# Kernel tuning notes

Measured on AMD Instinct MI355X. Metric: run time of the kernel, lower is better.

Reference implementation:

```python
import jax, jax.numpy as jnp
import numpy as np

T = 8192        # total tokens
HID = 2048      # hidden_size
H = 16          # num heads
D = 128         # head_dim
INNER = H * D   # 2048
CHUNK = 128
EPS = 1e-5
SCALE = D ** -0.5
ROPE_BASE = 600000.0


def _rmsnorm(x, w, eps=EPS):
    # x: [..., d]
    var = jnp.mean(jnp.square(x), axis=-1, keepdims=True)
    return x * jax.lax.rsqrt(var + eps) * w


def _rope(x, positions):
    # neox-style rope on full head_dim. x: [T, H, D], positions: [T]
    half = D // 2
    inv_freq = 1.0 / (ROPE_BASE ** (jnp.arange(half, dtype=jnp.float32) / half))
    ang = positions.astype(jnp.float32)[:, None] * inv_freq          # [T, half]
    cos = jnp.cos(ang)[:, None, :]                                   # [T, 1, half]
    sin = jnp.sin(ang)[:, None, :]
    x1, x2 = x[..., :half], x[..., half:]
    return jnp.concatenate([x1 * cos - x2 * sin, x2 * cos + x1 * sin], axis=-1)


def setup_inputs() -> dict:
    key = jax.random.key(0)
    ks = jax.random.split(key, 5)
    hidden_states = jax.random.normal(ks[0], (T, HID), dtype=jnp.float32)
    positions = jnp.arange(T, dtype=jnp.int64 if jax.config.jax_enable_x64 else jnp.int32)
    Wqkv = jax.random.normal(ks[1], (HID, 3 * INNER), dtype=jnp.float32) * 0.02
    q_ln_w = jnp.ones((D,), dtype=jnp.float32)
    k_ln_w = jnp.ones((D,), dtype=jnp.float32)
    Wg = jax.random.normal(ks[2], (HID, INNER), dtype=jnp.float32) * 0.02
    g_norm_w = jnp.ones((INNER,), dtype=jnp.float32)
    Wo = jax.random.normal(ks[3], (INNER, HID), dtype=jnp.float32) * 0.02
    return {"hidden_states": hidden_states, "positions": positions, "Wqkv": Wqkv,
            "q_ln_w": q_ln_w, "k_ln_w": k_ln_w, "Wg": Wg,
            "g_norm_w": g_norm_w, "Wo": Wo}


def reference(hidden_states, positions, Wqkv, q_ln_w, k_ln_w, Wg, g_norm_w, Wo):
    x = hidden_states.astype(jnp.float32)
    qkv = jax.nn.silu(x @ Wqkv)                                  # linear_silu=True, fp32
    q, k, v = jnp.split(qkv, [INNER, 2 * INNER], axis=-1)
    # per-head QK RMSNorm
    q = _rmsnorm(q.reshape(T, H, D), q_ln_w)
    k = _rmsnorm(k.reshape(T, H, D), k_ln_w)
    # rope
    q = _rope(q, positions)
    k = _rope(k, positions)
    v = v.reshape(T, H, D)
    q = q * SCALE  # scaling passed to RadixAttention

    # chunked causal linear attention: o_t = q_t @ sum_{s<=t} k_s v_s^T
    N = T // CHUNK
    qc = q.reshape(N, CHUNK, H, D)
    kc = k.reshape(N, CHUNK, H, D)
    vc = v.reshape(N, CHUNK, H, D)
    mask = jnp.tril(jnp.ones((CHUNK, CHUNK), dtype=jnp.float32))  # causal within chunk

    def step(S, chunk):
        qi, ki, vi = chunk                                        # [C, H, D]
        scores = jnp.einsum('chd,shd->hcs', qi, ki) * mask        # intra-chunk causal
        o = jnp.einsum('hcs,shd->chd', scores, vi)
        o = o + jnp.einsum('chd,hde->che', qi, S)                 # inter-chunk state
        S = S + jnp.einsum('chd,che->hde', ki, vi)
        return S, o

    S0 = jnp.zeros((H, D, D), dtype=jnp.float32)
    _, o = jax.lax.scan(step, S0, (qc, kc, vc))                   # o: [N, C, H, D]
    o = o.reshape(T, INNER)

    gate = x @ Wg                                                 # g_proj
    normed = _rmsnorm(o, g_norm_w)                                # group_norm_size == 1
    gated = jax.nn.sigmoid(gate) * normed
    return gated @ Wo                                             # out proj (no bias)
```

## Files before the change

kernel.cpp:

```cpp
#include <hip/hip_runtime.h>
#include <cstdint>
#include <cstddef>

typedef unsigned short u16;
typedef __attribute__((ext_vector_type(8))) short short8;
typedef __attribute__((ext_vector_type(4))) float f32x4;

#define T_SEQ 8192
#define NH 16
#define HD 128
#define NCH 64
#define KDIM 2048

constexpr float EPS = 1e-5f;
constexpr float SCALE = 0.08838834764831845f;

__device__ __forceinline__ u16 f2bf(float f) {
  union { float f; unsigned u; } v; v.f = f;
  unsigned r = v.u + 0x7fffu + ((v.u >> 16) & 1u);
  return (u16)(r >> 16);
}
__device__ __forceinline__ float bf2f(u16 h) {
  union { unsigned u; float f; } v; v.u = ((unsigned)h) << 16;
  return v.f;
}
__device__ __forceinline__ f32x4 mfma16(short8 a, short8 b, f32x4 c) {
  return __builtin_amdgcn_mfma_f32_16x16x32_bf16(a, b, c, 0, 0, 0);
}
__device__ __forceinline__ void gl2lds(const u16* g, u16* l) {
  __builtin_amdgcn_global_load_lds(
      (const __attribute__((address_space(1))) void*)g,
      (__attribute__((address_space(3))) void*)l, 16, 0, 0);
}

__global__ __launch_bounds__(256) void cast_f32_bf16(const float* __restrict__ src,
                                                     u16* __restrict__ dst, long n) {
  long i = ((long)blockIdx.x * 256 + threadIdx.x) * 8;
  if (i >= n) return;
  float4 a = *(const float4*)(src + i);
  float4 b = *(const float4*)(src + i + 4);
  alignas(16) u16 u[8] = {f2bf(a.x), f2bf(a.y), f2bf(a.z), f2bf(a.w),
                          f2bf(b.x), f2bf(b.y), f2bf(b.z), f2bf(b.w)};
  *(int4*)(dst + i) = *(const int4*)u;
}

__global__ __launch_bounds__(256) void transpose_cast(const float* __restrict__ W,
                                                      u16* __restrict__ Wt, int K, int N) {
  __shared__ u16 tile[64][72];
  int n0 = blockIdx.x * 64, k0 = blockIdx.y * 64;
  int tx = threadIdx.x, ty = threadIdx.y;
  for (int r = ty; r < 64; r += 4)
    tile[r][tx] = f2bf(W[(size_t)(k0 + r) * N + n0 + tx]);
  __syncthreads();
  for (int r = ty; r < 64; r += 4)
    Wt[(size_t)(n0 + r) * K + k0 + tx] = tile[tx][r];
}

template <int EPI>
__global__ __launch_bounds__(512) void gemm256(const u16* __restrict__ A,
                                               const u16* __restrict__ Bt, int N,
                                               float* __restrict__ Cf,
                                               u16* __restrict__ Cb,
                                               u16* __restrict__ q_t,
                                               u16* __restrict__ k_t,
                                               u16* __restrict__ v_t) {
  __shared__ u16 lds[65536];
  const int tid  = threadIdx.x;
  const int wave = tid >> 6, lane = tid & 63;
  const int lr = lane & 15, lg = lane >> 4;
  const int wr = wave >> 2, wc = wave & 3;
  const int bm = blockIdx.y, bn = blockIdx.x;
  const int sx  = (lr & 7) << 4;
  const int cu0 = ((lg * 16) ^ sx) >> 1;
  const int cu1 = ((64 + lg * 16) ^ sx) >> 1;

  const int srow  = tid >> 3;
  const int sslot = (tid & 7) ^ (srow & 7);
  const u16* gA = A  + (size_t)(bm * 256 + srow) * KDIM + sslot * 8;
  const u16* gB = Bt + (size_t)(bn * 256 + srow) * KDIM + sslot * 8;
  const int sbase = wave * 512;

  f32x4 acc[8][4];
  #pragma unroll
  for (int i = 0; i < 8; i++)
    #pragma unroll
    for (int j = 0; j < 4; j++) acc[i][j] = (f32x4){0.f, 0.f, 0.f, 0.f};

  auto STAGE = [&](int op, int buf, int half, int kt) {
    const u16* g = (op ? gB : gA) + (size_t)half * 128 * KDIM + kt * 64;
    u16* l = &lds[buf * 32768 + op * 16384 + half * 8192 + sbase];
    gl2lds(g, l);
    gl2lds(g + (size_t)64 * KDIM, l + 4096);
  };

  const int aoff = (wr * 64 + lr) * 64;
  const int boff = 16384 + (wc * 32 + lr) * 64;

  STAGE(0, 0, 0, 0); STAGE(1, 0, 0, 0); STAGE(0, 0, 1, 0); STAGE(1, 0, 1, 0);
  STAGE(0, 1, 0, 1); STAGE(1, 1, 1, 1); STAGE(0, 1, 1, 1);
  asm volatile("s_waitcnt vmcnt(6)" ::: "memory");
  __builtin_amdgcn_s_barrier();

  short8 af[4][2], b0f[2][2], b1f[2][2];
  const int NT = KDIM / 64;
  for (int t = 0; t < NT; ++t) {
    const int cur = t & 1, nxt = cur ^ 1;
    const int cb = cur * 32768;
    #pragma unroll
    for (int i = 0; i < 4; i++) {
      af[i][0] = *(const short8*)&lds[cb + aoff + i * 1024 + cu0];
      af[i][1] = *(const short8*)&lds[cb + aoff + i * 1024 + cu1];
    }
    #pragma unroll
    for (int j = 0; j < 2; j++) {
      b0f[j][0] = *(const short8*)&lds[cb + boff + j * 1024 + cu0];
      b0f[j][1] = *(const short8*)&lds[cb + boff + j * 1024 + cu1];
    }
    if (t + 1 < NT) STAGE(1, nxt, 0, t + 1);
    __builtin_amdgcn_s_barrier();
    asm volatile("s_waitcnt lgkmcnt(0)" ::: "memory");
    __builtin_amdgcn_s_setprio(1);
    #pragma unroll
    for (int i = 0; i < 4; i++)
      #pragma unroll
      for (int j = 0; j < 2; j++) {
        acc[i][j] = mfma16(af[i][0], b0f[j][0], acc[i][j]);
        acc[i][j] = mfma16(af[i][1], b0f[j][1], acc[i][j]);
      }
    __builtin_amdgcn_s_setprio(0);
    __builtin_amdgcn_s_barrier();
    #pragma unroll
    for (int j = 0; j < 2; j++) {
      b1f[j][0] = *(const short8*)&lds[cb + 8192 + boff + j * 1024 + cu0];
      b1f[j][1] = *(const short8*)&lds[cb + 8192 + boff + j * 1024 + cu1];
    }
    if (t + 2 < NT) STAGE(0, cur, 0, t + 2);
    __builtin_amdgcn_s_barrier();
    asm volatile("s_waitcnt lgkmcnt(0)" ::: "memory");
    __builtin_amdgcn_s_setprio(1);
    #pragma unroll
    for (int i = 0; i < 4; i++)
      #pragma unroll
      for (int j = 0; j < 2; j++) {
        acc[i][2 + j] = mfma16(af[i][0], b1f[j][0], acc[i][2 + j]);
        acc[i][2 + j] = mfma16(af[i][1], b1f[j][1], acc[i][2 + j]);
      }
    __builtin_amdgcn_s_setprio(0);
    __builtin_amdgcn_s_barrier();
    #pragma unroll
    for (int i = 0; i < 4; i++) {
      af[i][0] = *(const short8*)&lds[cb + 8192 + aoff + i * 1024 + cu0];
      af[i][1] = *(const short8*)&lds[cb + 8192 + aoff + i * 1024 + cu1];
    }
    if (t + 2 < NT) STAGE(1, cur, 1, t + 2);
    __builtin_amdgcn_s_barrier();
    asm volatile("s_waitcnt lgkmcnt(0)" ::: "memory");
    __builtin_amdgcn_s_setprio(1);
    #pragma unroll
    for (int i = 0; i < 4; i++)
      #pragma unroll
      for (int j = 0; j < 2; j++) {
        acc[4 + i][2 + j] = mfma16(af[i][0], b1f[j][0], acc[4 + i][2 + j]);
        acc[4 + i][2 + j] = mfma16(af[i][1], b1f[j][1], acc[4 + i][2 + j]);
      }
    __builtin_amdgcn_s_setprio(0);
    __builtin_amdgcn_s_barrier();
    if (t + 2 < NT) STAGE(0, cur, 1, t + 2);
    __builtin_amdgcn_s_barrier();
    asm volatile("s_waitcnt lgkmcnt(0)" ::: "memory");
    __builtin_amdgcn_s_setprio(1);
    #pragma unroll
    for (int i = 0; i < 4; i++)
      #pragma unroll
      for (int j = 0; j < 2; j++) {
        acc[4 + i][j] = mfma16(af[i][0], b0f[j][0], acc[4 + i][j]);
        acc[4 + i][j] = mfma16(af[i][1], b0f[j][1], acc[4 + i][j]);
      }
    __builtin_amdgcn_s_setprio(0);
    if (t + 2 < NT) asm volatile("s_waitcnt vmcnt(6)" ::: "memory");
    else            asm volatile("s_waitcnt vmcnt(0)" ::: "memory");
    __builtin_amdgcn_s_barrier();
  }

  #pragma unroll
  for (int mi = 0; mi < 8; mi++)
    #pragma unroll
    for (int nj = 0; nj < 4; nj++)
      #pragma unroll
      for (int r = 0; r < 4; r++) {
        int row = bm * 256 + (mi >> 2) * 128 + wr * 64 + (mi & 3) * 16 + lg * 4 + r;
        int col = bn * 256 + (nj >> 1) * 128 + wc * 32 + (nj & 1) * 16 + lr;
        float v = acc[mi][nj][r];
        if (EPI == 0) {
          Cf[(size_t)row * N + col] = v;
        } else if (EPI == 1) {
          Cb[(size_t)row * N + col] = f2bf(v);
        } else {
          float s = v / (1.0f + __expf(-v));
          int part = col >> 11;
          int h = (col >> 7) & 15;
          int d = col & 127;
          u16* dst = part == 0 ? q_t : (part == 1 ? k_t : v_t);
          dst[((size_t)h * T_SEQ + row) * HD + d] = f2bf(s);
        }
      }
}

__global__ __launch_bounds__(128) void qk_prep(u16* __restrict__ q_t, u16* __restrict__ k_t,
                                               const int* __restrict__ positions,
                                               const float* __restrict__ q_ln_w,
                                               const float* __restrict__ k_ln_w) {
  const int t = blockIdx.x, h = blockIdx.y, d = threadIdx.x;
  const size_t base = ((size_t)h * T_SEQ + t) * HD + d;
  float qv = bf2f(q_t[base]), kv = bf2f(k_t[base]);
  float s1 = qv * qv, s2 = kv * kv;
  #pragma unroll
  for (int off = 32; off > 0; off >>= 1) {
    s1 += __shfl_xor(s1, off);
    s2 += __shfl_xor(s2, off);
  }
  __shared__ float sh[4];
  if ((d & 63) == 0) { sh[(d >> 6) * 2] = s1; sh[(d >> 6) * 2 + 1] = s2; }
  __syncthreads();
  s1 = sh[0] + sh[2];
  s2 = sh[1] + sh[3];
  float rq = rsqrtf(s1 * (1.0f / 128.0f) + EPS);
  float rk = rsqrtf(s2 * (1.0f / 128.0f) + EPS);
  float qn = qv * rq * q_ln_w[d];
  float kn = kv * rk * k_ln_w[d];
  __shared__ float qsh[128], ksh[128];
  qsh[d] = qn; ksh[d] = kn;
  __syncthreads();
  int i = d & 63;
  float invf = exp2f((float)i * (-19.194593f / 64.0f));
  float ang = (float)positions[t] * invf;
  float cv = cosf(ang), sv = sinf(ang);
  float q2 = qsh[d ^ 64], k2 = ksh[d ^ 64];
  float qr = (d < 64) ? (qn * cv - q2 * sv) : (qn * cv + q2 * sv);
  float kr = (d < 64) ? (kn * cv - k2 * sv) : (kn * cv + k2 * sv);
  q_t[base] = f2bf(qr * SCALE);
  k_t[base] = f2bf(kr);
}

__global__ __launch_bounds__(256) void attn_phaseB(const u16* __restrict__ k_t,
                                                   const u16* __restrict__ v_t,
                                                   u16* __restrict__ G) {
  const int c = blockIdx.x, h = blockIdx.y;
  __shared__ u16 lV[128 * 72];
  __shared__ u16 lK[128 * 72];
  const int tid = threadIdx.x, wave = tid >> 6, lane = tid & 63;
  const int wm = (wave >> 1) * 64, wn = (wave & 1) * 64;
  const int lr = lane & 15, lg = lane >> 4;
  f32x4 acc[4][4];
  #pragma unroll
  for (int i = 0; i < 4; i++)
    #pragma unroll
    for (int j = 0; j < 4; j++) acc[i][j] = (f32x4){0.f, 0.f, 0.f, 0.f};

  const int tr = tid >> 2, seg = (tid & 3) * 32;
  for (int h2 = 0; h2 < 2; h2++) {
    __syncthreads();
    const u16* vsrc = v_t + ((size_t)h * T_SEQ + c * 128 + h2 * 64 + tr) * HD + seg;
    const u16* ksrc = k_t + ((size_t)h * T_SEQ + c * 128 + h2 * 64 + tr) * HD + seg;
    #pragma unroll
    for (int m = 0; m < 32; m += 8) {
      int4 rv = *(const int4*)(vsrc + m);
      int4 rk = *(const int4*)(ksrc + m);
      const u16* ev = (const u16*)&rv;
      const u16* ek = (const u16*)&rk;
      #pragma unroll
      for (int j = 0; j < 8; j++) {
        lV[(seg + m + j) * 72 + tr] = ev[j];
        lK[(seg + m + j) * 72 + tr] = ek[j];
      }
    }
    __syncthreads();
    #pragma unroll
    for (int kk = 0; kk < 64; kk += 32) {
      short8 af[4], bfr[4];
      #pragma unroll
      for (int i = 0; i < 4; i++)
        af[i] = *(const short8*)&lV[(wm + i * 16 + lr) * 72 + kk + lg * 8];
      #pragma unroll
      for (int j = 0; j < 4; j++)
        bfr[j] = *(const short8*)&lK[(wn + j * 16 + lr) * 72 + kk + lg * 8];
      #pragma unroll
      for (int i = 0; i < 4; i++)
        #pragma unroll
        for (int j = 0; j < 4; j++)
          acc[i][j] = mfma16(af[i], bfr[j], acc[i][j]);
    }
  }
  u16* Gp = G + ((size_t)h * NCH + c) * 16384;
  #pragma unroll
  for (int i = 0; i < 4; i++)
    #pragma unroll
    for (int j = 0; j < 4; j++)
      #pragma unroll
      for (int r = 0; r < 4; r++)
        Gp[(wm + i * 16 + lg * 4 + r) * 128 + wn + j * 16 + lr] = f2bf(acc[i][j][r]);
}

__global__ __launch_bounds__(256) void prefix_S(u16* __restrict__ G) {
  long idx = (long)blockIdx.x * 256 + threadIdx.x;
  int h = (int)(idx >> 14);
  int ed = (int)(idx & 16383);
  float run = 0.f;
  size_t base = (size_t)h * NCH * 16384 + ed;
  for (int c = 0; c < NCH; c++) {
    float g = bf2f(G[base + (size_t)c * 16384]);
    G[base + (size_t)c * 16384] = f2bf(run);
    run += g;
  }
}

__global__ __launch_bounds__(256) void attn_phaseC(const u16* __restrict__ q_t,
                                                   const u16* __restrict__ k_t,
                                                   const u16* __restrict__ v_t,
                                                   const u16* __restrict__ G,
                                                   u16* __restrict__ o_bf) {
  const int c = blockIdx.x, h = blockIdx.y;
  __shared__ u16 lP[128 * 136];
  __shared__ u16 lV[128 * 72];
  const int tid = threadIdx.x, wave = tid >> 6, lane = tid & 63;
  const int wm = wave * 32;
  const int lr = lane & 15, lg = lane >> 4;

  f32x4 acc1[2][8], acc2[2][8];
  #pragma unroll
  for (int i = 0; i < 2; i++)
    #pragma unroll
    for (int j = 0; j < 8; j++) {
      acc1[i][j] = (f32x4){0.f, 0.f, 0.f, 0.f};
      acc2[i][j] = (f32x4){0.f, 0.f, 0.f, 0.f};
    }

  const u16* Sp = G + ((size_t)h * NCH + c) * 16384;
  const u16* qbase = q_t + ((size_t)h * T_SEQ + c * 128) * HD;
  const u16* kbase = k_t + ((size_t)h * T_SEQ + c * 128) * HD;

  #pragma unroll
  for (int kk = 0; kk < 128; kk += 32) {
    short8 af[2];
    #pragma unroll
    for (int i = 0; i < 2; i++)
      af[i] = *(const short8*)(qbase + (wm + i * 16 + lr) * HD + kk + lg * 8);
    #pragma unroll
    for (int j = 0; j < 8; j++) {
      short8 bK = *(const short8*)(kbase + (j * 16 + lr) * HD + kk + lg * 8);
      short8 bS = *(const short8*)(Sp + (j * 16 + lr) * 128 + kk + lg * 8);
      #pragma unroll
      for (int i = 0; i < 2; i++) {
        acc1[i][j] = mfma16(af[i], bK, acc1[i][j]);
        acc2[i][j] = mfma16(af[i], bS, acc2[i][j]);
      }
    }
  }
  #pragma unroll
  for (int i = 0; i < 2; i++)
    #pragma unroll
    for (int j = 0; j < 8; j++)
      #pragma unroll
      for (int r = 0; r < 4; r++) {
        int row = wm + i * 16 + lg * 4 + r;
        int col = j * 16 + lr;
        float v = (col <= row) ? acc1[i][j][r] : 0.0f;
        lP[row * 136 + col] = f2bf(v);
      }

  const int tr = tid >> 2, seg = (tid & 3) * 32;
  for (int sh2 = 0; sh2 < 2; sh2++) {
    __syncthreads();
    const u16* vsrc = v_t + ((size_t)h * T_SEQ + c * 128 + sh2 * 64 + tr) * HD + seg;
    #pragma unroll
    for (int m = 0; m < 32; m += 8) {
      int4 rv = *(const int4*)(vsrc + m);
      const u16* ev = (const u16*)&rv;
      #pragma unroll
      for (int j = 0; j < 8; j++) lV[(seg + m + j) * 72 + tr] = ev[j];
    }
    __syncthreads();
    #pragma unroll
    for (int kk = 0; kk < 64; kk += 32) {
      short8 af[2];
      #pragma unroll
      for (int i = 0; i < 2; i++)
        af[i] = *(const short8*)&lP[(wm + i * 16 + lr) * 136 + sh2 * 64 + kk + lg * 8];
      #pragma unroll
      for (int j = 0; j < 8; j++) {
        short8 bV = *(const short8*)&lV[(j * 16 + lr) * 72 + kk + lg * 8];
        #pragma unroll
        for (int i = 0; i < 2; i++)
          acc2[i][j] = mfma16(af[i], bV, acc2[i][j]);
      }
    }
  }
  #pragma unroll
  for (int i = 0; i < 2; i++)
    #pragma unroll
    for (int j = 0; j < 8; j++)
      #pragma unroll
      for (int r = 0; r < 4; r++) {
        int row = wm + i * 16 + lg * 4 + r;
        int e = j * 16 + lr;
        o_bf[(size_t)(c * 128 + row) * 2048 + h * 128 + e] = f2bf(acc2[i][j][r]);
      }
}

__global__ __launch_bounds__(256) void gated_kernel(const u16* __restrict__ o_bf,
                                                    const u16* __restrict__ gate_bf,
                                                    const float* __restrict__ g_norm_w,
                                                    u16* __restrict__ gated_bf) {
  const int t = blockIdx.x, tid = threadIdx.x;
  const u16* orow = o_bf + (size_t)t * 2048;
  float vals[8], ss = 0.f;
  #pragma unroll
  for (int j = 0; j < 8; j++) {
    float v = bf2f(orow[tid + j * 256]);
    vals[j] = v;
    ss += v * v;
  }
  #pragma unroll
  for (int off = 32; off > 0; off >>= 1) ss += __shfl_xor(ss, off);
  __shared__ float sh[4];
  if ((tid & 63) == 0) sh[tid >> 6] = ss;
  __syncthreads();
  ss = sh[0] + sh[1] + sh[2] + sh[3];
  float r = rsqrtf(ss * (1.0f / 2048.0f) + EPS);
  const u16* grow = gate_bf + (size_t)t * 2048;
  u16* drow = gated_bf + (size_t)t * 2048;
  #pragma unroll
  for (int j = 0; j < 8; j++) {
    int col = tid + j * 256;
    float normed = vals[j] * r * g_norm_w[col];
    float g = bf2f(grow[col]);
    float sg = 1.0f / (1.0f + __expf(-g));
    drow[col] = f2bf(normed * sg);
  }
}

extern "C" void kernel_launch(void* const* d_in, const int* in_sizes, int n_in,
                              void* d_out, int out_size, void* d_ws, size_t ws_size,
                              hipStream_t stream) {
  const float* x = (const float*)d_in[0];
  const int* positions = (const int*)d_in[1];
  const float* Wqkv = (const float*)d_in[2];
  const float* q_ln_w = (const float*)d_in[3];
  const float* k_ln_w = (const float*)d_in[4];
  const float* Wg = (const float*)d_in[5];
  const float* g_norm_w = (const float*)d_in[6];
  const float* Wo = (const float*)d_in[7];
  float* out = (float*)d_out;

  char* ws = (char*)d_ws;
  const size_t M32 = (size_t)32 * 1024 * 1024;
  u16* WqkvT   = (u16*)ws;
  u16* G       = (u16*)ws;
  u16* gate_bf = (u16*)ws;
  u16* WgT     = (u16*)(ws + M32);
  u16* q_t     = (u16*)(ws + M32 + 8388608);
  u16* x_bf2   = q_t;
  u16* gated   = q_t;
  u16* k_t     = (u16*)(ws + M32 + 8388608 + M32);
  u16* WoT     = k_t;
  u16* v_t     = (u16*)(ws + M32 + 8388608 + 2 * M32);
  u16* x_bf    = (u16*)(ws + M32 + 8388608 + 3 * M32);
  u16* o_bf    = x_bf;
  const size_t needed = M32 + 8388608 + 4 * M32;
  if (ws_size < needed) return;

  cast_f32_bf16<<<8192, 256, 0, stream>>>(x, x_bf, (long)8192 * 2048);
  transpose_cast<<<dim3(96, 32), dim3(64, 4), 0, stream>>>(Wqkv, WqkvT, 2048, 6144);
  transpose_cast<<<dim3(32, 32), dim3(64, 4), 0, stream>>>(Wg, WgT, 2048, 2048);

  gemm256<2><<<dim3(24, 32), 512, 0, stream>>>(x_bf, WqkvT, 6144, nullptr, nullptr, q_t, k_t, v_t);

  qk_prep<<<dim3(8192, 16), 128, 0, stream>>>(q_t, k_t, positions, q_ln_w, k_ln_w);

  attn_phaseB<<<dim3(64, 16), 256, 0, stream>>>(k_t, v_t, G);
  prefix_S<<<1024, 256, 0, stream>>>(G);
  attn_phaseC<<<dim3(64, 16), 256, 0, stream>>>(q_t, k_t, v_t, G, o_bf);

  cast_f32_bf16<<<8192, 256, 0, stream>>>(x, x_bf2, (long)8192 * 2048);
  gemm256<1><<<dim3(8, 64 / 2), 512, 0, stream>>>(x_bf2, WgT, 2048, nullptr, gate_bf, nullptr, nullptr, nullptr);
  gated_kernel<<<8192, 256, 0, stream>>>(o_bf, gate_bf, g_norm_w, gated);

  transpose_cast<<<dim3(32, 32), dim3(64, 4), 0, stream>>>(Wo, WoT, 2048, 2048);
  gemm256<0><<<dim3(8, 32), 512, 0, stream>>>(gated, WoT, 2048, out, nullptr, nullptr, nullptr, nullptr);
}
```

Measured before the change: 682.9 us.

## Vectorize elementwise kernels, drop redundant x cast, write attention output head-major

qk_prep now handles two elements per lane and uses warp shuffles instead of shared memory and block barriers. LDS transpose stores in the attention kernels and the prefix scan are packed into wider stores. The second fp32-to-bf16 cast of x is removed so the gate GEMM reuses the first cast buffer. The attention output is written head-major in place over the state buffer, and gated_kernel reads and writes it with 16-byte accesses. In exchange, the workspace aliasing is reshuffled, which depends on the in-place read-then-write order staying correct.

```diff
diff --git a/kernel.cpp b/kernel.cpp
--- a/kernel.cpp
+++ b/kernel.cpp
@@ -23,6 +23,9 @@
 __device__ __forceinline__ float bf2f(u16 h) {
   union { unsigned u; float f; } v; v.u = ((unsigned)h) << 16;
   return v.f;
+}
+__device__ __forceinline__ unsigned pack2(u16 a, u16 b) {
+  return (unsigned)a | ((unsigned)b << 16);
 }
 __device__ __forceinline__ f32x4 mfma16(short8 a, short8 b, f32x4 c) {
   return __builtin_amdgcn_mfma_f32_16x16x32_bf16(a, b, c, 0, 0, 0);
@@ -206,40 +209,47 @@
       }
 }
 
-__global__ __launch_bounds__(128) void qk_prep(u16* __restrict__ q_t, u16* __restrict__ k_t,
+__global__ __launch_bounds__(256) void qk_prep(u16* __restrict__ q_t, u16* __restrict__ k_t,
                                                const int* __restrict__ positions,
                                                const float* __restrict__ q_ln_w,
                                                const float* __restrict__ k_ln_w) {
-  const int t = blockIdx.x, h = blockIdx.y, d = threadIdx.x;
-  const size_t base = ((size_t)h * T_SEQ + t) * HD + d;
-  float qv = bf2f(q_t[base]), kv = bf2f(k_t[base]);
-  float s1 = qv * qv, s2 = kv * kv;
+  const int t = blockIdx.x;
+  const int h = blockIdx.y * 4 + (threadIdx.x >> 6);
+  const int lane = threadIdx.x & 63;
+  const int d0 = lane * 2;
+  const size_t base = ((size_t)h * T_SEQ + t) * HD + d0;
+  unsigned qu = *(const unsigned*)(q_t + base);
+  unsigned ku = *(const unsigned*)(k_t + base);
+  float q0 = bf2f((u16)qu), q1 = bf2f((u16)(qu >> 16));
+  float k0 = bf2f((u16)ku), k1 = bf2f((u16)(ku >> 16));
+  float s1 = q0 * q0 + q1 * q1;
+  float s2 = k0 * k0 + k1 * k1;
   #pragma unroll
   for (int off = 32; off > 0; off >>= 1) {
     s1 += __shfl_xor(s1, off);
     s2 += __shfl_xor(s2, off);
   }
-  __shared__ float sh[4];
-  if ((d & 63) == 0) { sh[(d >> 6) * 2] = s1; sh[(d >> 6) * 2 + 1] = s2; }
-  __syncthreads();
-  s1 = sh[0] + sh[2];
-  s2 = sh[1] + sh[3];
   float rq = rsqrtf(s1 * (1.0f / 128.0f) + EPS);
   float rk = rsqrtf(s2 * (1.0f / 128.0f) + EPS);
-  float qn = qv * rq * q_ln_w[d];
-  float kn = kv * rk * k_ln_w[d];
-  __shared__ float qsh[128], ksh[128];
-  qsh[d] = qn; ksh[d] = kn;
-  __syncthreads();
-  int i = d & 63;
-  float invf = exp2f((float)i * (-19.194593f / 64.0f));
-  float ang = (float)positions[t] * invf;
-  float cv = cosf(ang), sv = sinf(ang);
-  float q2 = qsh[d ^ 64], k2 = ksh[d ^ 64];
-  float qr = (d < 64) ? (qn * cv - q2 * sv) : (qn * cv + q2 * sv);
-  float kr = (d < 64) ? (kn * cv - k2 * sv) : (kn * cv + k2 * sv);
-  q_t[base] = f2bf(qr * SCALE);
-  k_t[base] = f2bf(kr);
+  float w0 = q_ln_w[d0], w1 = q_ln_w[d0 + 1];
+  float u0 = k_ln_w[d0], u1 = k_ln_w[d0 + 1];
+  float qn0 = q0 * rq * w0, qn1 = q1 * rq * w1;
+  float kn0 = k0 * rk * u0, kn1 = k1 * rk * u1;
+  float qp0 = __shfl_xor(qn0, 32), qp1 = __shfl_xor(qn1, 32);
+  float kp0 = __shfl_xor(kn0, 32), kp1 = __shfl_xor(kn1, 32);
+  int i0 = d0 & 63;
+  float invf0 = exp2f((float)i0 * (-19.194593f / 64.0f));
+  float invf1 = exp2f((float)(i0 + 1) * (-19.194593f / 64.0f));
+  float pos = (float)positions[t];
+  float a0 = pos * invf0, a1 = pos * invf1;
+  float c0 = cosf(a0), sn0 = sinf(a0), c1 = cosf(a1), sn1 = sinf(a1);
+  bool lo = lane < 32;
+  float qr0 = lo ? (qn0 * c0 - qp0 * sn0) : (qn0 * c0 + qp0 * sn0);
+  float qr1 = lo ? (qn1 * c1 - qp1 * sn1) : (qn1 * c1 + qp1 * sn1);
+  float kr0 = lo ? (kn0 * c0 - kp0 * sn0) : (kn0 * c0 + kp0 * sn0);
+  float kr1 = lo ? (kn1 * c1 - kp1 * sn1) : (kn1 * c1 + kp1 * sn1);
+  *(unsigned*)(q_t + base) = pack2(f2bf(qr0 * SCALE), f2bf(qr1 * SCALE));
+  *(unsigned*)(k_t + base) = pack2(f2bf(kr0), f2bf(kr1));
 }
 
 __global__ __launch_bounds__(256) void attn_phaseB(const u16* __restrict__ k_t,
@@ -257,22 +267,29 @@
     #pragma unroll
     for (int j = 0; j < 4; j++) acc[i][j] = (f32x4){0.f, 0.f, 0.f, 0.f};
 
-  const int tr = tid >> 2, seg = (tid & 3) * 32;
+  const int t0 = (tid >> 4) * 4;
+  const int ds = (tid & 15) * 8;
   for (int h2 = 0; h2 < 2; h2++) {
     __syncthreads();
-    const u16* vsrc = v_t + ((size_t)h * T_SEQ + c * 128 + h2 * 64 + tr) * HD + seg;
-    const u16* ksrc = k_t + ((size_t)h * T_SEQ + c * 128 + h2 * 64 + tr) * HD + seg;
-    #pragma unroll
-    for (int m = 0; m < 32; m += 8) {
-      int4 rv = *(const int4*)(vsrc + m);
-      int4 rk = *(const int4*)(ksrc + m);
-      const u16* ev = (const u16*)&rv;
-      const u16* ek = (const u16*)&rk;
-      #pragma unroll
-      for (int j = 0; j < 8; j++) {
-        lV[(seg + m + j) * 72 + tr] = ev[j];
-        lK[(seg + m + j) * 72 + tr] = ek[j];
-      }
+    const u16* vsrc = v_t + ((size_t)h * T_SEQ + c * 128 + h2 * 64 + t0) * HD + ds;
+    const u16* ksrc = k_t + ((size_t)h * T_SEQ + c * 128 + h2 * 64 + t0) * HD + ds;
+    int4 rv[4], rk[4];
+    #pragma unroll
+    for (int r = 0; r < 4; r++) {
+      rv[r] = *(const int4*)(vsrc + r * HD);
+      rk[r] = *(const int4*)(ksrc + r * HD);
+    }
+    const u16* v0 = (const u16*)&rv[0]; const u16* v1 = (const u16*)&rv[1];
+    const u16* v2 = (const u16*)&rv[2]; const u16* v3 = (const u16*)&rv[3];
+    const u16* K0 = (const u16*)&rk[0]; const u16* K1 = (const u16*)&rk[1];
+    const u16* K2 = (const u16*)&rk[2]; const u16* K3 = (const u16*)&rk[3];
+    #pragma unroll
+    for (int j = 0; j < 8; j++) {
+      uint2 wv, wk;
+      wv.x = pack2(v0[j], v1[j]); wv.y = pack2(v2[j], v3[j]);
+      wk.x = pack2(K0[j], K1[j]); wk.y = pack2(K2[j], K3[j]);
+      *(uint2*)&lV[(ds + j) * 72 + t0] = wv;
+      *(uint2*)&lK[(ds + j) * 72 + t0] = wk;
     }
     __syncthreads();
     #pragma unroll
@@ -302,15 +319,20 @@
 }
 
 __global__ __launch_bounds__(256) void prefix_S(u16* __restrict__ G) {
-  long idx = (long)blockIdx.x * 256 + threadIdx.x;
-  int h = (int)(idx >> 14);
-  int ed = (int)(idx & 16383);
-  float run = 0.f;
-  size_t base = (size_t)h * NCH * 16384 + ed;
+  int idx = blockIdx.x * 256 + threadIdx.x;
+  int h = idx >> 12;
+  int e4 = (idx & 4095) * 4;
+  float run0 = 0.f, run1 = 0.f, run2 = 0.f, run3 = 0.f;
+  size_t base = (size_t)h * NCH * 16384 + e4;
   for (int c = 0; c < NCH; c++) {
-    float g = bf2f(G[base + (size_t)c * 16384]);
-    G[base + (size_t)c * 16384] = f2bf(run);
-    run += g;
+    uint2 g = *(uint2*)&G[base + (size_t)c * 16384];
+    float a0 = bf2f((u16)g.x), a1 = bf2f((u16)(g.x >> 16));
+    float a2 = bf2f((u16)g.y), a3 = bf2f((u16)(g.y >> 16));
+    uint2 o;
+    o.x = pack2(f2bf(run0), f2bf(run1));
+    o.y = pack2(f2bf(run2), f2bf(run3));
+    *(uint2*)&G[base + (size_t)c * 16384] = o;
+    run0 += a0; run1 += a1; run2 += a2; run3 += a3;
   }
 }
 
@@ -318,7 +340,7 @@
                                                    const u16* __restrict__ k_t,
                                                    const u16* __restrict__ v_t,
                                                    const u16* __restrict__ G,
-                                                   u16* __restrict__ o_bf) {
+                                                   u16* __restrict__ o_hm) {
   const int c = blockIdx.x, h = blockIdx.y;
   __shared__ u16 lP[128 * 136];
   __shared__ u16 lV[128 * 72];
@@ -368,16 +390,21 @@
         lP[row * 136 + col] = f2bf(v);
       }
 
-  const int tr = tid >> 2, seg = (tid & 3) * 32;
+  const int t0 = (tid >> 4) * 4;
+  const int ds = (tid & 15) * 8;
   for (int sh2 = 0; sh2 < 2; sh2++) {
     __syncthreads();
-    const u16* vsrc = v_t + ((size_t)h * T_SEQ + c * 128 + sh2 * 64 + tr) * HD + seg;
-    #pragma unroll
-    for (int m = 0; m < 32; m += 8) {
-      int4 rv = *(const int4*)(vsrc + m);
-      const u16* ev = (const u16*)&rv;
-      #pragma unroll
-      for (int j = 0; j < 8; j++) lV[(seg + m + j) * 72 + tr] = ev[j];
+    const u16* vsrc = v_t + ((size_t)h * T_SEQ + c * 128 + sh2 * 64 + t0) * HD + ds;
+    int4 rv[4];
+    #pragma unroll
+    for (int r = 0; r < 4; r++) rv[r] = *(const int4*)(vsrc + r * HD);
+    const u16* v0 = (const u16*)&rv[0]; const u16* v1 = (const u16*)&rv[1];
+    const u16* v2 = (const u16*)&rv[2]; const u16* v3 = (const u16*)&rv[3];
+    #pragma unroll
+    for (int j = 0; j < 8; j++) {
+      uint2 wv;
+      wv.x = pack2(v0[j], v1[j]); wv.y = pack2(v2[j], v3[j]);
+      *(uint2*)&lV[(ds + j) * 72 + t0] = wv;
     }
     __syncthreads();
     #pragma unroll
@@ -395,6 +422,7 @@
       }
     }
   }
+  u16* op = o_hm + ((size_t)h * NCH + c) * 16384;
   #pragma unroll
   for (int i = 0; i < 2; i++)
     #pragma unroll
@@ -403,20 +431,23 @@
       for (int r = 0; r < 4; r++) {
         int row = wm + i * 16 + lg * 4 + r;
         int e = j * 16 + lr;
-        o_bf[(size_t)(c * 128 + row) * 2048 + h * 128 + e] = f2bf(acc2[i][j][r]);
-      }
-}
-
-__global__ __launch_bounds__(256) void gated_kernel(const u16* __restrict__ o_bf,
+        op[row * 128 + e] = f2bf(acc2[i][j][r]);
+      }
+}
+
+__global__ __launch_bounds__(256) void gated_kernel(const u16* __restrict__ o_hm,
                                                     const u16* __restrict__ gate_bf,
                                                     const float* __restrict__ g_norm_w,
                                                     u16* __restrict__ gated_bf) {
   const int t = blockIdx.x, tid = threadIdx.x;
-  const u16* orow = o_bf + (size_t)t * 2048;
+  const int h = tid >> 4, e0 = (tid & 15) * 8;
+  const int c = t >> 7, row = t & 127;
+  short8 ov = *(const short8*)(o_hm + (((size_t)h * NCH + c) * 128 + row) * 128 + e0);
+  const u16* ovp = (const u16*)&ov;
   float vals[8], ss = 0.f;
   #pragma unroll
   for (int j = 0; j < 8; j++) {
-    float v = bf2f(orow[tid + j * 256]);
+    float v = bf2f(ovp[j]);
     vals[j] = v;
     ss += v * v;
   }
@@ -427,16 +458,20 @@
   __syncthreads();
   ss = sh[0] + sh[1] + sh[2] + sh[3];
   float r = rsqrtf(ss * (1.0f / 2048.0f) + EPS);
-  const u16* grow = gate_bf + (size_t)t * 2048;
-  u16* drow = gated_bf + (size_t)t * 2048;
+  short8 gv = *(const short8*)(gate_bf + (size_t)t * 2048 + tid * 8);
+  const u16* gvp = (const u16*)&gv;
+  float4 w0 = *(const float4*)(g_norm_w + tid * 8);
+  float4 w1 = *(const float4*)(g_norm_w + tid * 8 + 4);
+  float wv[8] = {w0.x, w0.y, w0.z, w0.w, w1.x, w1.y, w1.z, w1.w};
+  alignas(16) u16 outu[8];
   #pragma unroll
   for (int j = 0; j < 8; j++) {
-    int col = tid + j * 256;
-    float normed = vals[j] * r * g_norm_w[col];
-    float g = bf2f(grow[col]);
+    float normed = vals[j] * r * wv[j];
+    float g = bf2f(gvp[j]);
     float sg = 1.0f / (1.0f + __expf(-g));
-    drow[col] = f2bf(normed * sg);
-  }
+    outu[j] = f2bf(normed * sg);
+  }
+  *(int4*)(gated_bf + (size_t)t * 2048 + tid * 8) = *(const int4*)outu;
 }
 
 extern "C" void kernel_launch(void* const* d_in, const int* in_sizes, int n_in,
@@ -456,16 +491,14 @@
   const size_t M32 = (size_t)32 * 1024 * 1024;
   u16* WqkvT   = (u16*)ws;
   u16* G       = (u16*)ws;
-  u16* gate_bf = (u16*)ws;
   u16* WgT     = (u16*)(ws + M32);
   u16* q_t     = (u16*)(ws + M32 + 8388608);
-  u16* x_bf2   = q_t;
   u16* gated   = q_t;
   u16* k_t     = (u16*)(ws + M32 + 8388608 + M32);
-  u16* WoT     = k_t;
+  u16* gate_bf = k_t;
   u16* v_t     = (u16*)(ws + M32 + 8388608 + 2 * M32);
+  u16* WoT     = v_t;
   u16* x_bf    = (u16*)(ws + M32 + 8388608 + 3 * M32);
-  u16* o_bf    = x_bf;
   const size_t needed = M32 + 8388608 + 4 * M32;
   if (ws_size < needed) return;
 
@@ -475,15 +508,14 @@
 
   gemm256<2><<<dim3(24, 32), 512, 0, stream>>>(x_bf, WqkvT, 6144, nullptr, nullptr, q_t, k_t, v_t);
 
-  qk_prep<<<dim3(8192, 16), 128, 0, stream>>>(q_t, k_t, positions, q_ln_w, k_ln_w);
+  qk_prep<<<dim3(8192, 4), 256, 0, stream>>>(q_t, k_t, positions, q_ln_w, k_ln_w);
 
   attn_phaseB<<<dim3(64, 16), 256, 0, stream>>>(k_t, v_t, G);
-  prefix_S<<<1024, 256, 0, stream>>>(G);
-  attn_phaseC<<<dim3(64, 16), 256, 0, stream>>>(q_t, k_t, v_t, G, o_bf);
-
-  cast_f32_bf16<<<8192, 256, 0, stream>>>(x, x_bf2, (long)8192 * 2048);
-  gemm256<1><<<dim3(8, 64 / 2), 512, 0, stream>>>(x_bf2, WgT, 2048, nullptr, gate_bf, nullptr, nullptr, nullptr);
-  gated_kernel<<<8192, 256, 0, stream>>>(o_bf, gate_bf, g_norm_w, gated);
+  prefix_S<<<256, 256, 0, stream>>>(G);
+  attn_phaseC<<<dim3(64, 16), 256, 0, stream>>>(q_t, k_t, v_t, G, G);
+
+  gemm256<1><<<dim3(8, 32), 512, 0, stream>>>(x_bf, WgT, 2048, nullptr, gate_bf, nullptr, nullptr, nullptr);
+  gated_kernel<<<8192, 256, 0, stream>>>(G, gate_bf, g_norm_w, gated);
 
   transpose_cast<<<dim3(32, 32), dim3(64, 4), 0, stream>>>(Wo, WoT, 2048, 2048);
   gemm256<0><<<dim3(8, 32), 512, 0, stream>>>(gated, WoT, 2048, out, nullptr, nullptr, nullptr, nullptr);
```

Measured after the change: 650.4 us. 1.05x faster.
